# Kernel optimization log

Measured on AMD Instinct MI355X. Metric: run time of the kernel, lower is better.

Reference implementation:

```python
import jax, jax.numpy as jnp
from jax import lax
import numpy as np

# ---- hyperparams (match init_kwargs) ----
NUM_HASHES = 8
BITS = 5
TABLE_SIZE = 64
M = 27            # ALSH augmentation length; M % (KH*KW) == 0
U = 0.83
KH = KW = 3
STRIDE = 1
PAD = 1
OUT_CHANNELS = 256
IN_CHANNELS = 64


def setup_inputs() -> dict:
    key = jax.random.key(0)
    k1, k2, k3 = jax.random.split(key, 3)
    x = jax.random.normal(k1, (32, IN_CHANNELS, 56, 56), jnp.float32)
    kernels = jax.random.normal(k2, (OUT_CHANNELS, IN_CHANNELS, KH, KW), jnp.float32) * 0.05
    a = jax.random.normal(k3, (NUM_HASHES * BITS, IN_CHANNELS * KH * KW + M), jnp.float32)
    return {"x": x, "kernels": kernels, "a": a}


def _scale_under_U(kv):
    # ScaleUnder_U: rescale all kernel vectors so max L2 norm == U
    norms = jnp.sqrt(jnp.sum(kv * kv, axis=1))
    return kv * (U / jnp.max(norms))


def _P(kv):
    # ALSH preprocessing: append ||x||^2, ||x||^4, ..., ||x||^(2^M)
    p = jnp.sum(kv * kv, axis=1, keepdims=True)  # ||x||^2
    cols = []
    for _ in range(M):
        cols.append(p)
        p = p * p
    return jnp.concatenate([kv] + cols, axis=1)  # [K, D+M]


_BIT_W = (2 ** jnp.arange(BITS)).astype(jnp.int32)


def _hash_vectors(a, v):
    # v: [K, D+M] -> bucket indices [NUM_HASHES, K]
    proj = v @ a.T                                   # [K, NUM_HASHES*BITS]
    bits = (proj > 0).astype(jnp.int32).reshape(-1, NUM_HASHES, BITS)
    idx = jnp.einsum('khb,b->hk', bits, _BIT_W)      # multi-bit SRP index
    return idx % TABLE_SIZE


def _build_table(bucket):
    # vectorized equivalent of the nested scalar-scatter loops in init_table:
    # append kernel id i to table[bucket[h, i]] in (h-major, i-minor) order.
    H, K = bucket.shape
    flat = bucket.reshape(-1)                        # [H*K]
    vals = (jnp.arange(H * K) % K).astype(jnp.int32) # stored value = kernel index i
    order = jnp.argsort(flat)                        # stable in jax
    sb, sv = flat[order], vals[order]
    pos = jnp.arange(H * K) - jnp.searchsorted(sb, sb, side='left')  # slot within bucket
    row_len = H * K
    table = jnp.zeros((TABLE_SIZE, row_len), jnp.int32).at[sb, pos].set(sv)
    lengths = jnp.zeros((TABLE_SIZE,), jnp.int32).at[flat].add(1)
    return table, lengths


def _vote_buckets(x, a):
    # Q: append M/(KH*KW) constant 1/2 planes; hash via convolution with a reshaped
    N, C, H, W = x.shape
    m_planes = M // (KH * KW)
    xq = jnp.concatenate([x, jnp.full((N, m_planes, H, W), 0.5, x.dtype)], axis=1)
    hk = a.reshape(NUM_HASHES * BITS, C + m_planes, KH, KW)  # a_to_kernel
    d = lax.conv_general_dilated(xq, hk, (STRIDE, STRIDE), [(PAD, PAD), (PAD, PAD)],
                                 dimension_numbers=('NCHW', 'OIHW', 'NCHW'))
    # [N, NUM_HASHES*BITS, H', W'] -> bucket per (hash fn, location)
    Np, _, Hp, Wp = d.shape
    bits = (d > 0).astype(jnp.int32).reshape(Np, NUM_HASHES, BITS, Hp * Wp)
    buckets = jnp.einsum('nhbs,b->hns', bits, _BIT_W) % TABLE_SIZE  # [H, N, S]
    return buckets.reshape(NUM_HASHES, -1)


def _active_mask(x, kernels, a):
    K = kernels.shape[0]
    kv = kernels.reshape(K, -1)
    buckets_k = _hash_vectors(a, _P(_scale_under_U(kv)))   # [H, K]
    table, lengths = _build_table(buckets_k)
    votes = _vote_buckets(x, a)                            # [H, N*S]
    tallied = jnp.zeros((NUM_HASHES, TABLE_SIZE), jnp.int32).at[
        jnp.arange(NUM_HASHES)[:, None], votes].add(1)     # count_votes
    indices = jnp.argmax(tallied, axis=1)                  # best bucket per hash fn
    entries = table[indices]                               # [H, row_len]
    valid = jnp.arange(table.shape[1])[None, :] < lengths[indices][:, None]
    # union of kernel ids across selected buckets (== sort+unique gather)
    mask = jnp.zeros((K,), jnp.float32).at[entries.reshape(-1)].max(
        valid.reshape(-1).astype(jnp.float32))
    return mask, tallied, indices


def reference(x, kernels, a):
    mask, tallied, indices = _active_mask(x, kernels, a)
    out = lax.conv_general_dilated(x, kernels, (STRIDE, STRIDE), [(PAD, PAD), (PAD, PAD)],
                                   dimension_numbers=('NCHW', 'OIHW', 'NCHW'))
    out = out * mask[None, :, None, None]  # conv restricted to the active kernel set
    return out, tallied, indices, mask
```

## Files before the change

kernel.cpp:

```cpp
#include <hip/hip_runtime.h>
#include <math.h>

#define NH 8
#define BITS_ 5
#define NB 40
#define TS 64
#define MAUG 27
#define CIN 64
#define HH 56
#define WW 56
#define NN 32
#define OCH 256
#define DK 576
#define DPM 603
#define HW (HH*WW)

#define UST 59
#define LO_OFF 7552
#define SMEM_DW 15104

typedef __attribute__((ext_vector_type(4))) float f32x4;
typedef __attribute__((ext_vector_type(8))) _Float16 f16x8;
typedef union { uint4 u; f16x8 h; } fragh_u;

__device__ __forceinline__ unsigned int f16b(float v) {
    union { _Float16 h; unsigned short u; } cv;
    cv.h = (_Float16)v;
    return (unsigned int)cv.u;
}
__device__ __forceinline__ float f16tof(unsigned int b) {
    union { _Float16 h; unsigned short u; } cv;
    cv.u = (unsigned short)b;
    return (float)cv.h;
}

__global__ void kP(const float* __restrict__ kern, const float* __restrict__ a,
                   float* __restrict__ aT, float* __restrict__ ctab,
                   int* __restrict__ tallied, float* __restrict__ normP,
                   unsigned short* __restrict__ whA,
                   unsigned short* __restrict__ vaH, unsigned short* __restrict__ vaL)
{
    const int bid = blockIdx.x;
    const int t = threadIdx.x;
    if (bid < 32) {
        for (int idx = bid * 256 + t; idx < DPM * NB; idx += 32 * 256) {
            int d = idx / NB, j = idx - d * NB;
            aT[idx] = a[j * DPM + d];
        }
    } else if (bid == 32) {
        for (int g = t; g < 9 * NB; g += 256) {
            int pat = g / NB, j = g - pat * NB;
            int ry = pat / 3, rx = pat % 3;
            float s = 0.f;
            for (int ky = 0; ky < 3; ++ky) {
                if (ry == 0 && ky == 0) continue;
                if (ry == 2 && ky == 2) continue;
                for (int kx = 0; kx < 3; ++kx) {
                    if (rx == 0 && kx == 0) continue;
                    if (rx == 2 && kx == 2) continue;
                    for (int mc = 0; mc < 3; ++mc)
                        s += a[j * DPM + DK + mc * 9 + ky * 3 + kx];
                }
            }
            ctab[g] = 0.5f * s;
        }
        for (int g = t; g < NH * TS; g += 256) tallied[g] = 0;
    } else if (bid < 37) {
        int g = (bid - 33) * 256 + t;
        int oc = g >> 2, part = g & 3;
        const float4* p = (const float4*)(kern + oc * DK + part * 144);
        float sq = 0.f;
        #pragma unroll 4
        for (int i = 0; i < 36; ++i) {
            float4 v = p[i];
            sq += v.x * v.x + v.y * v.y + v.z * v.z + v.w * v.w;
        }
        normP[g] = sq;
    } else {
        int idx = (bid - 37) * 256 + t;
        int f = idx >> 6, lane = idx & 63;
        if (f < 288) {
            const int kidxG = f >> 4, mf = f & 15;
            const int tap = kidxG % 9, cc = kidxG / 9;
            const int oc = mf * 16 + (lane & 15);
            const int cbase = cc * 32 + (lane >> 4) * 8;
            unsigned int hs[8];
            #pragma unroll
            for (int j = 0; j < 8; ++j)
                hs[j] = f16b(kern[oc * DK + (cbase + j) * 9 + tap]);
            unsigned int* p = (unsigned int*)(whA + ((size_t)f * 64 + lane) * 8);
            #pragma unroll
            for (int w2 = 0; w2 < 4; ++w2)
                p[w2] = hs[2 * w2] | (hs[2 * w2 + 1] << 16);
        } else if (f < 342) {
            const int fv = f - 288;
            const int kidxG = fv / 3, mfv = fv % 3;
            const int tap = kidxG % 9, cc = kidxG / 9;
            const int j = mfv * 16 + (lane & 15);
            const int cbase = cc * 32 + (lane >> 4) * 8;
            unsigned int hs[8], ls[8];
            #pragma unroll
            for (int jj = 0; jj < 8; ++jj) {
                float w = (j < NB) ? a[j * DPM + (cbase + jj) * 9 + tap] : 0.f;
                unsigned int h = f16b(w);
                unsigned int l = f16b(w - f16tof(h));
                hs[jj] = h; ls[jj] = l;
            }
            unsigned int* ph = (unsigned int*)(vaH + ((size_t)fv * 64 + lane) * 8);
            unsigned int* pl = (unsigned int*)(vaL + ((size_t)fv * 64 + lane) * 8);
            #pragma unroll
            for (int w2 = 0; w2 < 4; ++w2) {
                ph[w2] = hs[2 * w2] | (hs[2 * w2 + 1] << 16);
                pl[w2] = ls[2 * w2] | (ls[2 * w2 + 1] << 16);
            }
        }
    }
}

__global__ void __launch_bounds__(256) kH(const float* __restrict__ kern,
        const float* __restrict__ aT, const float* __restrict__ normP,
        int* __restrict__ bucket_k)
{
    __shared__ float xs[DK];
    __shared__ float red[256];
    __shared__ float accR[3 * 41];
    __shared__ float proj[NB];
    const int t = threadIdx.x;
    const int lane = t & 63, ty = t >> 6;
    const int oc = blockIdx.x;

    red[t] = fmaxf(fmaxf(normP[t], normP[t + 256]), fmaxf(normP[t + 512], normP[t + 768]));
    __syncthreads();
    for (int s = 128; s > 0; s >>= 1) {
        if (t < s) red[t] = fmaxf(red[t], red[t + s]);
        __syncthreads();
    }
    const float scale = 0.83f / sqrtf(red[0]);
    for (int i = t; i < DK; i += 256) xs[i] = scale * kern[(size_t)oc * DK + i];
    __syncthreads();

    const int j = (lane < NB) ? lane : (NB - 1);
    float acc = 0.f, sq = 0.f;
    const int d0 = ty * 144;
    for (int d = d0; d < d0 + 144; ++d) {
        float xv = xs[d];
        sq += xv * xv;
        acc += xv * aT[d * NB + j];
    }
    if (ty > 0) {
        if (lane < NB) accR[(ty - 1) * 41 + lane] = acc;
        if (lane == NB) accR[(ty - 1) * 41 + 40] = sq;
    }
    __syncthreads();
    if (ty == 0 && lane < NB) {
        acc += (accR[lane] + accR[41 + lane]) + accR[82 + lane];
        sq += (accR[40] + accR[81]) + accR[122];
        float pv = sq;
        for (int m = 0; m < MAUG; ++m) {
            acc += pv * aT[(DK + m) * NB + lane];
            pv = pv * pv;
        }
        proj[lane] = acc;
    }
    __syncthreads();
    if (t < NH) {
        int b = 0;
        #pragma unroll
        for (int bb = 0; bb < BITS_; ++bb)
            if (proj[t * BITS_ + bb] > 0.f) b |= (1 << bb);
        bucket_k[t * OCH + oc] = b & (TS - 1);
    }
}

#define ADX(kidx, nb) ((rowu + ((((kidx) % 9) / 3) * 8 + ((kidx) / 9) * 4) * UST + (nb) + (((kidx) % 9) % 3)) * 4)

__global__ void __launch_bounds__(512, 4) kM(const float* __restrict__ x,
        const unsigned short* __restrict__ whA,
        const unsigned short* __restrict__ vaH, const unsigned short* __restrict__ vaL,
        const float* __restrict__ ctab, int* __restrict__ tallied,
        float* __restrict__ out)
{
    __shared__ unsigned int smem[SMEM_DW];
    const int lane = threadIdx.x, wid = threadIdx.y;
    const int id = blockIdx.y * 28 + blockIdx.x;
    const int swz = (id & 7) * 112 + (id >> 3);
    const int n = swz / 28;
    const int y0 = (swz - n * 28) * 2;
    const int lcol = lane & 15, hi4 = lane >> 4;
    const int t = wid * 64 + lane;
    const int mg = wid & 3, ng = wid >> 2;
    const int colbase = (mg == 3) ? 40 : mg * 16;
    const uint4* wbase = (const uint4*)whA + (size_t)mg * 4 * 64 + lane;
    const int rowu = (ng * 8 + hi4) * UST + lcol;

    fragh_u ahA[4], ahB[4];
    #pragma unroll
    for (int mf = 0; mf < 4; ++mf) ahA[mf].u = wbase[mf * 64];

    {
        const int r = wid & 3, half = wid >> 2;
        const int y = y0 - 1 + r;
        const bool valid = (lane < WW) && (y >= 0) && (y < HH);
        const int colc = (lane < WW) ? lane : (WW - 1);
        const int yc = (y >= 0 && y < HH) ? y : 0;
        const float* xb = x + (((size_t)n * CIN + half * 32) * HH + yc) * WW + colc;
        float xv[32];
        #pragma unroll
        for (int i = 0; i < 32; ++i) xv[i] = xb[(size_t)i * HW];

        if (t < 256) {
            const int tile = t >> 7, rem = t & 127;
            const int L = (rem & 1) ? 57 : 0;
            const int u = (rem >> 1) & 7, rr = rem >> 4;
            *(uint4*)&smem[tile * LO_OFF + ((rr * 8 + u) * UST + L) * 4] =
                make_uint4(0u, 0u, 0u, 0u);
        }

        #pragma unroll
        for (int uu = 0; uu < 4; ++uu) {
            unsigned int dh[4], dl[4];
            #pragma unroll
            for (int dd = 0; dd < 4; ++dd) {
                float v0 = valid ? xv[uu * 8 + dd * 2] : 0.f;
                float v1 = valid ? xv[uu * 8 + dd * 2 + 1] : 0.f;
                unsigned int h0 = f16b(v0), h1 = f16b(v1);
                unsigned int l0 = f16b(v0 - f16tof(h0));
                unsigned int l1 = f16b(v1 - f16tof(h1));
                dh[dd] = h0 | (h1 << 16);
                dl[dd] = l0 | (l1 << 16);
            }
            if (lane < WW) {
                const int ad = ((r * 8 + half * 4 + uu) * UST + 1 + lane) * 4;
                *(uint4*)&smem[ad] = make_uint4(dh[0], dh[1], dh[2], dh[3]);
                *(uint4*)&smem[LO_OFF + ad] = make_uint4(dl[0], dl[1], dl[2], dl[3]);
            }
        }
    }
    __syncthreads();

    {
        f32x4 acc[4][4];
        #pragma unroll
        for (int mf = 0; mf < 4; ++mf)
            #pragma unroll
            for (int nf = 0; nf < 4; ++nf)
                acc[mf][nf] = (f32x4){0.f, 0.f, 0.f, 0.f};

        fragh_u bhP[3];
        bhP[0].u = *(const uint4*)&smem[ADX(0, 0)];
        bhP[1].u = *(const uint4*)&smem[ADX(0, 16)];

        #pragma unroll
        for (int step = 0; step < 72; ++step) {
            const int kidx = step >> 2, nf = step & 3;
            fragh_u* cur = (kidx & 1) ? ahB : ahA;
            fragh_u* nxt = (kidx & 1) ? ahA : ahB;
            if (nf == 0 && kidx < 17) {
                #pragma unroll
                for (int mf = 0; mf < 4; ++mf)
                    nxt[mf].u = wbase[(kidx + 1) * 1024 + mf * 64];
            }
            if (step + 2 < 72) {
                const int s2 = step + 2;
                const int k2 = s2 >> 2, nf2 = s2 & 3;
                const int nb2 = (nf2 == 3) ? 40 : nf2 * 16;
                bhP[s2 % 3].u = *(const uint4*)&smem[ADX(k2, nb2)];
            }
            const fragh_u bh = bhP[step % 3];
            __builtin_amdgcn_s_setprio(1);
            acc[0][nf] = __builtin_amdgcn_mfma_f32_16x16x32_f16(cur[0].h, bh.h, acc[0][nf], 0, 0, 0);
            acc[1][nf] = __builtin_amdgcn_mfma_f32_16x16x32_f16(cur[1].h, bh.h, acc[1][nf], 0, 0, 0);
            acc[2][nf] = __builtin_amdgcn_mfma_f32_16x16x32_f16(cur[2].h, bh.h, acc[2][nf], 0, 0, 0);
            acc[3][nf] = __builtin_amdgcn_mfma_f32_16x16x32_f16(cur[3].h, bh.h, acc[3][nf], 0, 0, 0);
            __builtin_amdgcn_s_setprio(0);
        }

        const int yrow = y0 + ng;
        #pragma unroll
        for (int mf = 0; mf < 4; ++mf) {
            #pragma unroll
            for (int reg = 0; reg < 4; ++reg) {
                const int oc = (mg * 4 + mf) * 16 + hi4 * 4 + reg;
                float* ob = out + (((size_t)n * OCH + oc) * HH + yrow) * WW;
                #pragma unroll
                for (int nf = 0; nf < 4; ++nf) {
                    const int col = ((nf == 3) ? 40 : nf * 16) + lcol;
                    ob[col] = acc[mf][nf][reg];
                }
            }
        }
    }

    f32x4 vacc[3];
    vacc[0] = (f32x4){0.f, 0.f, 0.f, 0.f};
    vacc[1] = (f32x4){0.f, 0.f, 0.f, 0.f};
    vacc[2] = (f32x4){0.f, 0.f, 0.f, 0.f};
    {
        const uint4* vbH = (const uint4*)vaH + lane;
        const uint4* vbL = (const uint4*)vaL + lane;
        fragh_u vh[3], vl[3];
        fragh_u bhV[2], blV[2];
        vh[0].u = vbH[0];   vl[0].u = vbL[0];
        vh[1].u = vbH[64];  vl[1].u = vbL[64];
        bhV[0].u = *(const uint4*)&smem[ADX(0, colbase)];
        blV[0].u = *(const uint4*)&smem[LO_OFF + ADX(0, colbase)];
        #pragma unroll
        for (int s = 0; s < 54; ++s) {
            const int kidx = s / 3, mfv = s % 3;
            const int b = kidx & 1;
            if (s + 2 < 54) {
                vh[(s + 2) % 3].u = vbH[(s + 2) * 64];
                vl[(s + 2) % 3].u = vbL[(s + 2) * 64];
            }
            if (mfv == 0 && kidx < 17) {
                bhV[b ^ 1].u = *(const uint4*)&smem[ADX(kidx + 1, colbase)];
                blV[b ^ 1].u = *(const uint4*)&smem[LO_OFF + ADX(kidx + 1, colbase)];
            }
            const fragh_u vhc = vh[s % 3], vlc = vl[s % 3];
            __builtin_amdgcn_s_setprio(1);
            vacc[mfv] = __builtin_amdgcn_mfma_f32_16x16x32_f16(vhc.h, bhV[b].h, vacc[mfv], 0, 0, 0);
            vacc[mfv] = __builtin_amdgcn_mfma_f32_16x16x32_f16(vhc.h, blV[b].h, vacc[mfv], 0, 0, 0);
            vacc[mfv] = __builtin_amdgcn_mfma_f32_16x16x32_f16(vlc.h, bhV[b].h, vacc[mfv], 0, 0, 0);
            __builtin_amdgcn_s_setprio(0);
        }
    }

    __syncthreads();
    float* projT = (float*)smem;
    int* hist = (int*)&smem[6144];
    {
        const int px = colbase + lcol;
        #pragma unroll
        for (int mfv = 0; mfv < 3; ++mfv)
            #pragma unroll
            for (int reg = 0; reg < 4; ++reg)
                projT[(ng * 64 + px) * 49 + mfv * 16 + hi4 * 4 + reg] = vacc[mfv][reg];
    }
    hist[t] = 0;
    __syncthreads();
    if (t < 2 * WW) {
        const int row = t / WW, pxx = t - row * WW;
        const int yv = y0 + row;
        const int ry = (yv == 0) ? 0 : ((yv == HH - 1) ? 2 : 1);
        const int rx = (pxx == 0) ? 0 : ((pxx == WW - 1) ? 2 : 1);
        const float* ct = ctab + (ry * 3 + rx) * NB;
        const float* pr = projT + (row * 64 + pxx) * 49;
        #pragma unroll
        for (int h = 0; h < NH; ++h) {
            int b = 0;
            #pragma unroll
            for (int bb = 0; bb < BITS_; ++bb)
                if (pr[h * BITS_ + bb] + ct[h * BITS_ + bb] > 0.f) b |= (1 << bb);
            atomicAdd(&hist[h * TS + (b & (TS - 1))], 1);
        }
    }
    __syncthreads();
    {
        int v = hist[t];
        if (v) atomicAdd(&tallied[t], v);
    }
}

__global__ void __launch_bounds__(256) kCZ(const int* __restrict__ tallied,
        const int* __restrict__ bucket_k, float* __restrict__ o_tallied,
        float* __restrict__ o_indices, float* __restrict__ o_mask,
        float* __restrict__ out)
{
    __shared__ int s_idx[NH];
    __shared__ int s_mk;
    const int t = threadIdx.x;
    {
        const int h = t >> 5, j = t & 31;
        int v1 = tallied[h * TS + j], v2 = tallied[h * TS + 32 + j];
        int v, idx;
        if (v2 > v1) { v = v2; idx = 32 + j; } else { v = v1; idx = j; }
        #pragma unroll
        for (int s = 16; s > 0; s >>= 1) {
            int ov = __shfl_down(v, s, 32);
            int oi = __shfl_down(idx, s, 32);
            if (ov > v || (ov == v && oi < idx)) { v = ov; idx = oi; }
        }
        if (j == 0) s_idx[h] = idx;
    }
    __syncthreads();
    const int oc = blockIdx.x & (OCH - 1);
    const int n = blockIdx.x >> 8;
    if (t == 0) {
        int mk = 0;
        #pragma unroll
        for (int hp = 0; hp < NH; ++hp) {
            int b = bucket_k[hp * OCH + oc];
            #pragma unroll
            for (int h = 0; h < NH; ++h) mk |= (b == s_idx[h]) ? 1 : 0;
        }
        s_mk = mk;
    }
    if (blockIdx.x == 0) {
        for (int i = t; i < NH * TS; i += 256) o_tallied[i] = (float)tallied[i];
        if (t < NH) o_indices[t] = (float)s_idx[t];
        {
            int mk = 0;
            #pragma unroll
            for (int hp = 0; hp < NH; ++hp) {
                int b = bucket_k[hp * OCH + t];
                #pragma unroll
                for (int h = 0; h < NH; ++h) mk |= (b == s_idx[h]) ? 1 : 0;
            }
            o_mask[t] = (float)mk;
        }
    }
    __syncthreads();
    if (s_mk) return;
    float4* o = (float4*)(out + ((size_t)n * OCH + oc) * HW);
    for (int i = t; i < HW / 4; i += 256)
        o[i] = make_float4(0.f, 0.f, 0.f, 0.f);
}

extern "C" void kernel_launch(void* const* d_in, const int* in_sizes, int n_in,
                              void* d_out, int out_size, void* d_ws, size_t ws_size,
                              hipStream_t stream)
{
    const float* x    = (const float*)d_in[0];
    const float* kern = (const float*)d_in[1];
    const float* a    = (const float*)d_in[2];

    float* out       = (float*)d_out;
    float* o_tallied = out + (size_t)NN * OCH * HW;
    float* o_indices = o_tallied + NH * TS;
    float* o_mask    = o_indices + NH;

    float* ws = (float*)d_ws;
    float* aT       = ws;
    float* ctab     = ws + 24320;
    float* normP    = ws + 24704;
    int*   tallied  = (int*)(ws + 25728);
    int*   bucket_k = (int*)(ws + 26240);
    unsigned short* whA = (unsigned short*)(ws + 28544);
    unsigned short* vaH = (unsigned short*)(ws + 102272);
    unsigned short* vaL = (unsigned short*)(ws + 116096);

    kP<<<123, 256, 0, stream>>>(kern, a, aT, ctab, tallied, normP, whA, vaH, vaL);
    kH<<<OCH, 256, 0, stream>>>(kern, aT, normP, bucket_k);
    kM<<<dim3(28, NN), dim3(64, 8), 0, stream>>>(x, whA, vaH, vaL, ctab, tallied, out);
    kCZ<<<NN * OCH, 256, 0, stream>>>(tallied, bucket_k, o_tallied, o_indices, o_mask, out);
}
```

Before: 105.1 us.

## Halve kM row tile to one output row per block and split columns across waves

After: 118.3 us. 1.12x slower.

```diff
diff --git a/kernel.cpp b/kernel.cpp
--- a/kernel.cpp
+++ b/kernel.cpp
@@ -16,8 +16,8 @@
 #define HW (HH*WW)
 
 #define UST 59
-#define LO_OFF 7552
-#define SMEM_DW 15104
+#define LO_OFF 5664
+#define SMEM_DW 11328
 
 typedef __attribute__((ext_vector_type(4))) float f32x4;
 typedef __attribute__((ext_vector_type(8))) _Float16 f16x8;
@@ -172,9 +172,9 @@
     }
 }
 
-#define ADX(kidx, nb) ((rowu + ((((kidx) % 9) / 3) * 8 + ((kidx) / 9) * 4) * UST + (nb) + (((kidx) % 9) % 3)) * 4)
-
-__global__ void __launch_bounds__(512, 4) kM(const float* __restrict__ x,
+#define ADX(kidx, nb) ((((((kidx) % 9) / 3) * 8 + ((kidx) / 9) * 4 + hi4) * UST + (nb) + lcol + (((kidx) % 9) % 3)) * 4)
+
+__global__ void __launch_bounds__(512, 5) kM(const float* __restrict__ x,
         const unsigned short* __restrict__ whA,
         const unsigned short* __restrict__ vaH, const unsigned short* __restrict__ vaL,
         const float* __restrict__ ctab, int* __restrict__ tallied,
@@ -182,23 +182,24 @@
 {
     __shared__ unsigned int smem[SMEM_DW];
     const int lane = threadIdx.x, wid = threadIdx.y;
-    const int id = blockIdx.y * 28 + blockIdx.x;
-    const int swz = (id & 7) * 112 + (id >> 3);
-    const int n = swz / 28;
-    const int y0 = (swz - n * 28) * 2;
+    const int id = blockIdx.y * 56 + blockIdx.x;
+    const int swz = (id & 7) * 224 + (id >> 3);
+    const int n = swz / 56;
+    const int y0 = swz - n * 56;
     const int lcol = lane & 15, hi4 = lane >> 4;
     const int t = wid * 64 + lane;
-    const int mg = wid & 3, ng = wid >> 2;
+    const int mg = wid & 3, cg = wid >> 2;
     const int colbase = (mg == 3) ? 40 : mg * 16;
+    const int nbA = cg * 32;
+    const int nbB = cg * 32 + (cg ? 8 : 16);
     const uint4* wbase = (const uint4*)whA + (size_t)mg * 4 * 64 + lane;
-    const int rowu = (ng * 8 + hi4) * UST + lcol;
 
     fragh_u ahA[4], ahB[4];
     #pragma unroll
     for (int mf = 0; mf < 4; ++mf) ahA[mf].u = wbase[mf * 64];
 
-    {
-        const int r = wid & 3, half = wid >> 2;
+    if (wid < 6) {
+        const int r = wid >> 1, half = wid & 1;
         const int y = y0 - 1 + r;
         const bool valid = (lane < WW) && (y >= 0) && (y < HH);
         const int colc = (lane < WW) ? lane : (WW - 1);
@@ -207,15 +208,6 @@
         float xv[32];
         #pragma unroll
         for (int i = 0; i < 32; ++i) xv[i] = xb[(size_t)i * HW];
-
-        if (t < 256) {
-            const int tile = t >> 7, rem = t & 127;
-            const int L = (rem & 1) ? 57 : 0;
-            const int u = (rem >> 1) & 7, rr = rem >> 4;
-            *(uint4*)&smem[tile * LO_OFF + ((rr * 8 + u) * UST + L) * 4] =
-                make_uint4(0u, 0u, 0u, 0u);
-        }
-
         #pragma unroll
         for (int uu = 0; uu < 4; ++uu) {
             unsigned int dh[4], dl[4];
@@ -235,116 +227,144 @@
                 *(uint4*)&smem[LO_OFF + ad] = make_uint4(dl[0], dl[1], dl[2], dl[3]);
             }
         }
+    } else {
+        const int t2 = t - 384;
+        if (t2 < 96) {
+            const int L = (t2 & 1) ? 57 : 0;
+            const int u = (t2 >> 1) & 7;
+            const int rt = t2 >> 4;
+            const int r = rt % 3, tile = rt / 3;
+            *(uint4*)&smem[tile * LO_OFF + ((r * 8 + u) * UST + L) * 4] =
+                make_uint4(0u, 0u, 0u, 0u);
+        }
     }
     __syncthreads();
 
     {
-        f32x4 acc[4][4];
-        #pragma unroll
-        for (int mf = 0; mf < 4; ++mf)
-            #pragma unroll
-            for (int nf = 0; nf < 4; ++nf)
-                acc[mf][nf] = (f32x4){0.f, 0.f, 0.f, 0.f};
-
-        fragh_u bhP[3];
-        bhP[0].u = *(const uint4*)&smem[ADX(0, 0)];
-        bhP[1].u = *(const uint4*)&smem[ADX(0, 16)];
-
-        #pragma unroll
-        for (int step = 0; step < 72; ++step) {
-            const int kidx = step >> 2, nf = step & 3;
+        f32x4 acc[4][2];
+        #pragma unroll
+        for (int mf = 0; mf < 4; ++mf) {
+            acc[mf][0] = (f32x4){0.f, 0.f, 0.f, 0.f};
+            acc[mf][1] = (f32x4){0.f, 0.f, 0.f, 0.f};
+        }
+        fragh_u bhP[2][2];
+        bhP[0][0].u = *(const uint4*)&smem[ADX(0, nbA)];
+        bhP[0][1].u = *(const uint4*)&smem[ADX(0, nbB)];
+
+        #pragma unroll
+        for (int kidx = 0; kidx < 18; ++kidx) {
             fragh_u* cur = (kidx & 1) ? ahB : ahA;
             fragh_u* nxt = (kidx & 1) ? ahA : ahB;
-            if (nf == 0 && kidx < 17) {
+            const int b = kidx & 1;
+            if (kidx < 17) {
                 #pragma unroll
                 for (int mf = 0; mf < 4; ++mf)
                     nxt[mf].u = wbase[(kidx + 1) * 1024 + mf * 64];
-            }
-            if (step + 2 < 72) {
-                const int s2 = step + 2;
-                const int k2 = s2 >> 2, nf2 = s2 & 3;
-                const int nb2 = (nf2 == 3) ? 40 : nf2 * 16;
-                bhP[s2 % 3].u = *(const uint4*)&smem[ADX(k2, nb2)];
-            }
-            const fragh_u bh = bhP[step % 3];
-            __builtin_amdgcn_s_setprio(1);
-            acc[0][nf] = __builtin_amdgcn_mfma_f32_16x16x32_f16(cur[0].h, bh.h, acc[0][nf], 0, 0, 0);
-            acc[1][nf] = __builtin_amdgcn_mfma_f32_16x16x32_f16(cur[1].h, bh.h, acc[1][nf], 0, 0, 0);
-            acc[2][nf] = __builtin_amdgcn_mfma_f32_16x16x32_f16(cur[2].h, bh.h, acc[2][nf], 0, 0, 0);
-            acc[3][nf] = __builtin_amdgcn_mfma_f32_16x16x32_f16(cur[3].h, bh.h, acc[3][nf], 0, 0, 0);
-            __builtin_amdgcn_s_setprio(0);
-        }
-
-        const int yrow = y0 + ng;
+                bhP[b ^ 1][0].u = *(const uint4*)&smem[ADX(kidx + 1, nbA)];
+                bhP[b ^ 1][1].u = *(const uint4*)&smem[ADX(kidx + 1, nbB)];
+            }
+            #pragma unroll
+            for (int nf = 0; nf < 2; ++nf) {
+                const fragh_u bh = bhP[b][nf];
+                __builtin_amdgcn_s_setprio(1);
+                acc[0][nf] = __builtin_amdgcn_mfma_f32_16x16x32_f16(cur[0].h, bh.h, acc[0][nf], 0, 0, 0);
+                acc[1][nf] = __builtin_amdgcn_mfma_f32_16x16x32_f16(cur[1].h, bh.h, acc[1][nf], 0, 0, 0);
+                acc[2][nf] = __builtin_amdgcn_mfma_f32_16x16x32_f16(cur[2].h, bh.h, acc[2][nf], 0, 0, 0);
+                acc[3][nf] = __builtin_amdgcn_mfma_f32_16x16x32_f16(cur[3].h, bh.h, acc[3][nf], 0, 0, 0);
+                __builtin_amdgcn_s_setprio(0);
+            }
+        }
+
         #pragma unroll
         for (int mf = 0; mf < 4; ++mf) {
             #pragma unroll
             for (int reg = 0; reg < 4; ++reg) {
                 const int oc = (mg * 4 + mf) * 16 + hi4 * 4 + reg;
-                float* ob = out + (((size_t)n * OCH + oc) * HH + yrow) * WW;
-                #pragma unroll
-                for (int nf = 0; nf < 4; ++nf) {
-                    const int col = ((nf == 3) ? 40 : nf * 16) + lcol;
-                    ob[col] = acc[mf][nf][reg];
-                }
-            }
-        }
-    }
-
-    f32x4 vacc[3];
+                float* ob = out + (((size_t)n * OCH + oc) * HH + y0) * WW;
+                ob[nbA + lcol] = acc[mf][0][reg];
+                ob[nbB + lcol] = acc[mf][1][reg];
+            }
+        }
+    }
+
+    f32x4 vacc[2];
     vacc[0] = (f32x4){0.f, 0.f, 0.f, 0.f};
     vacc[1] = (f32x4){0.f, 0.f, 0.f, 0.f};
-    vacc[2] = (f32x4){0.f, 0.f, 0.f, 0.f};
     {
         const uint4* vbH = (const uint4*)vaH + lane;
         const uint4* vbL = (const uint4*)vaL + lane;
-        fragh_u vh[3], vl[3];
         fragh_u bhV[2], blV[2];
-        vh[0].u = vbH[0];   vl[0].u = vbL[0];
-        vh[1].u = vbH[64];  vl[1].u = vbL[64];
         bhV[0].u = *(const uint4*)&smem[ADX(0, colbase)];
         blV[0].u = *(const uint4*)&smem[LO_OFF + ADX(0, colbase)];
-        #pragma unroll
-        for (int s = 0; s < 54; ++s) {
-            const int kidx = s / 3, mfv = s % 3;
-            const int b = kidx & 1;
-            if (s + 2 < 54) {
-                vh[(s + 2) % 3].u = vbH[(s + 2) * 64];
-                vl[(s + 2) % 3].u = vbL[(s + 2) * 64];
-            }
-            if (mfv == 0 && kidx < 17) {
-                bhV[b ^ 1].u = *(const uint4*)&smem[ADX(kidx + 1, colbase)];
-                blV[b ^ 1].u = *(const uint4*)&smem[LO_OFF + ADX(kidx + 1, colbase)];
-            }
-            const fragh_u vhc = vh[s % 3], vlc = vl[s % 3];
-            __builtin_amdgcn_s_setprio(1);
-            vacc[mfv] = __builtin_amdgcn_mfma_f32_16x16x32_f16(vhc.h, bhV[b].h, vacc[mfv], 0, 0, 0);
-            vacc[mfv] = __builtin_amdgcn_mfma_f32_16x16x32_f16(vhc.h, blV[b].h, vacc[mfv], 0, 0, 0);
-            vacc[mfv] = __builtin_amdgcn_mfma_f32_16x16x32_f16(vlc.h, bhV[b].h, vacc[mfv], 0, 0, 0);
-            __builtin_amdgcn_s_setprio(0);
+        if (cg == 0) {
+            fragh_u vh[2][2], vl[2][2];
+            vh[0][0].u = vbH[0];  vl[0][0].u = vbL[0];
+            vh[0][1].u = vbH[64]; vl[0][1].u = vbL[64];
+            #pragma unroll
+            for (int kidx = 0; kidx < 18; ++kidx) {
+                const int b = kidx & 1;
+                if (kidx < 17) {
+                    bhV[b ^ 1].u = *(const uint4*)&smem[ADX(kidx + 1, colbase)];
+                    blV[b ^ 1].u = *(const uint4*)&smem[LO_OFF + ADX(kidx + 1, colbase)];
+                    vh[b ^ 1][0].u = vbH[((kidx + 1) * 3 + 0) * 64];
+                    vl[b ^ 1][0].u = vbL[((kidx + 1) * 3 + 0) * 64];
+                    vh[b ^ 1][1].u = vbH[((kidx + 1) * 3 + 1) * 64];
+                    vl[b ^ 1][1].u = vbL[((kidx + 1) * 3 + 1) * 64];
+                }
+                #pragma unroll
+                for (int ci = 0; ci < 2; ++ci) {
+                    __builtin_amdgcn_s_setprio(1);
+                    vacc[ci] = __builtin_amdgcn_mfma_f32_16x16x32_f16(vh[b][ci].h, bhV[b].h, vacc[ci], 0, 0, 0);
+                    vacc[ci] = __builtin_amdgcn_mfma_f32_16x16x32_f16(vh[b][ci].h, blV[b].h, vacc[ci], 0, 0, 0);
+                    vacc[ci] = __builtin_amdgcn_mfma_f32_16x16x32_f16(vl[b][ci].h, bhV[b].h, vacc[ci], 0, 0, 0);
+                    __builtin_amdgcn_s_setprio(0);
+                }
+            }
+        } else {
+            fragh_u vh[2], vl[2];
+            vh[0].u = vbH[2 * 64];  vl[0].u = vbL[2 * 64];
+            #pragma unroll
+            for (int kidx = 0; kidx < 18; ++kidx) {
+                const int b = kidx & 1;
+                if (kidx < 17) {
+                    bhV[b ^ 1].u = *(const uint4*)&smem[ADX(kidx + 1, colbase)];
+                    blV[b ^ 1].u = *(const uint4*)&smem[LO_OFF + ADX(kidx + 1, colbase)];
+                    vh[b ^ 1].u = vbH[((kidx + 1) * 3 + 2) * 64];
+                    vl[b ^ 1].u = vbL[((kidx + 1) * 3 + 2) * 64];
+                }
+                __builtin_amdgcn_s_setprio(1);
+                vacc[0] = __builtin_amdgcn_mfma_f32_16x16x32_f16(vh[b].h, bhV[b].h, vacc[0], 0, 0, 0);
+                vacc[0] = __builtin_amdgcn_mfma_f32_16x16x32_f16(vh[b].h, blV[b].h, vacc[0], 0, 0, 0);
+                vacc[0] = __builtin_amdgcn_mfma_f32_16x16x32_f16(vl[b].h, bhV[b].h, vacc[0], 0, 0, 0);
+                __builtin_amdgcn_s_setprio(0);
+            }
         }
     }
 
     __syncthreads();
     float* projT = (float*)smem;
-    int* hist = (int*)&smem[6144];
+    int* hist = (int*)&smem[3072];
     {
         const int px = colbase + lcol;
-        #pragma unroll
-        for (int mfv = 0; mfv < 3; ++mfv)
+        if (cg == 0) {
+            #pragma unroll
+            for (int ci = 0; ci < 2; ++ci)
+                #pragma unroll
+                for (int reg = 0; reg < 4; ++reg)
+                    projT[px * 49 + ci * 16 + hi4 * 4 + reg] = vacc[ci][reg];
+        } else {
             #pragma unroll
             for (int reg = 0; reg < 4; ++reg)
-                projT[(ng * 64 + px) * 49 + mfv * 16 + hi4 * 4 + reg] = vacc[mfv][reg];
+                projT[px * 49 + 32 + hi4 * 4 + reg] = vacc[0][reg];
+        }
     }
     hist[t] = 0;
     __syncthreads();
-    if (t < 2 * WW) {
-        const int row = t / WW, pxx = t - row * WW;
-        const int yv = y0 + row;
-        const int ry = (yv == 0) ? 0 : ((yv == HH - 1) ? 2 : 1);
-        const int rx = (pxx == 0) ? 0 : ((pxx == WW - 1) ? 2 : 1);
+    if (t < WW) {
+        const int ry = (y0 == 0) ? 0 : ((y0 == HH - 1) ? 2 : 1);
+        const int rx = (t == 0) ? 0 : ((t == WW - 1) ? 2 : 1);
         const float* ct = ctab + (ry * 3 + rx) * NB;
-        const float* pr = projT + (row * 64 + pxx) * 49;
+        const float* pr = projT + t * 49;
         #pragma unroll
         for (int h = 0; h < NH; ++h) {
             int b = 0;
@@ -441,6 +461,6 @@
 
     kP<<<123, 256, 0, stream>>>(kern, a, aT, ctab, tallied, normP, whA, vaH, vaL);
     kH<<<OCH, 256, 0, stream>>>(kern, aT, normP, bucket_k);
-    kM<<<dim3(28, NN), dim3(64, 8), 0, stream>>>(x, whA, vaH, vaL, ctab, tallied, out);
+    kM<<<dim3(56, NN), dim3(64, 8), 0, stream>>>(x, whA, vaH, vaL, ctab, tallied, out);
     kCZ<<<NN * OCH, 256, 0, stream>>>(tallied, bucket_k, o_tallied, o_indices, o_mask, out);
 }
```
